# Optimization experiments

Hardware: AMD Instinct MI355X
Metric: run time of the kernel (lower is better)

## Reference

```python
import jax, jax.numpy as jnp
import numpy as np

B, NA, NM, P, IN, H, OUT = 64, 49, 19, 128, 64, 64, 60
H2 = 2 * H  # feature dim after each GCN concat and for the global GAT


def setup_inputs() -> dict:
    key = jax.random.key(0)
    ks = iter(jax.random.split(key, 64))
    def rn(shape, s=0.05):
        return jax.random.normal(next(ks), shape, jnp.float32) * s
    inp = {
        'agent_feature': jax.random.normal(next(ks), (B, NA, IN), jnp.float32),
        'map_feature': jax.random.normal(next(ks), (P, B, NM, IN), jnp.float32),
        'map_mask': jnp.ones((B, P), jnp.int32),
    }
    for pfx in ('a', 'm'):  # agent / map SubNetwork params, 3 layers each
        dims = [IN, H2, H2]
        for i in range(3):
            inp[f'{pfx}w{i}'] = rn((dims[i], H))
            inp[f'{pfx}b{i}'] = jnp.zeros((H,), jnp.float32)
            inp[f'{pfx}g{i}'] = jnp.ones((H,), jnp.float32)   # LayerNorm gamma
            inp[f'{pfx}n{i}'] = jnp.zeros((H,), jnp.float32)  # LayerNorm beta
    inp['gat_fc_w'] = rn((H2, H2))
    inp['gat_attn_w'] = rn((2 * H2,))  # attn_fc over concat([z_src, z_dst])
    inp['mlp_w'] = rn((H2, OUT))
    inp['mlp_b'] = jnp.zeros((OUT,), jnp.float32)
    return inp


def _layer_norm(x, g, b):
    mu = jnp.mean(x, axis=-1, keepdims=True)
    var = jnp.mean((x - mu) ** 2, axis=-1, keepdims=True)
    return g * (x - mu) / jnp.sqrt(var + 1e-5) + b


def _neighbor_max(h):
    # max over all OTHER nodes of a complete digraph (no self loop).
    # top-2 trick per channel avoids materializing an [N,N,D] mailbox.
    top2 = jax.lax.top_k(jnp.swapaxes(h, -1, -2), 2)[0]  # [..., D, 2]
    m1 = top2[..., 0][..., None, :]  # [..., 1, D] global max
    m2 = top2[..., 1][..., None, :]  # [..., 1, D] second max
    return jnp.where(h == m1, m2, m1)


def _subnet(x, params):
    for W, b, g, be in params:
        h = jax.nn.relu(_layer_norm(x @ W + b, g, be))
        x = jnp.concatenate([h, _neighbor_max(h)], axis=-1)
    return x


def _forward(agent_feature, map_feature, ap, mp, gat_fc_w, gat_attn_w, mlp_w, mlp_b):
    a = _subnet(agent_feature, ap)        # [B, NA, 2H]
    m = _subnet(map_feature, mp)          # [P, B, NM, 2H]
    agent_poly = jnp.max(a, axis=1)       # [B, 2H]
    map_poly = jnp.max(m, axis=2)         # [P, B, 2H]
    feats = jnp.concatenate([agent_poly[None], map_poly], axis=0)  # [1+P, B, 2H]
    feats = jnp.swapaxes(feats, 0, 1)     # [B, Nn, 2H], node 0 = agent
    z = feats @ gat_fc_w                  # [B, Nn, 2H]
    s = z @ gat_attn_w[:H2]               # [B, Nn] source contribution
    d = z @ gat_attn_w[H2:]               # [B, Nn] destination contribution
    e = jax.nn.leaky_relu(s[:, :, None] + d[:, None, :], 0.01)  # edge i->j: [B, i, j]
    nn_ = feats.shape[1]
    e = jnp.where(jnp.eye(nn_, dtype=bool)[None], -jnp.inf, e)  # no self edges
    alpha = jax.nn.softmax(e, axis=1)     # segment softmax over sources per dst
    hg = jnp.einsum('bij,bid->bjd', alpha, z)  # weighted-sum message passing
    return hg[:, 0] @ mlp_w + mlp_b       # agent node readout: [B, OUT]


def reference(agent_feature, map_feature, map_mask,
              aw0, ab0, ag0, an0, aw1, ab1, ag1, an1, aw2, ab2, ag2, an2,
              mw0, mb0, mg0, mn0, mw1, mb1, mg1, mn1, mw2, mb2, mg2, mn2,
              gat_fc_w, gat_attn_w, mlp_w, mlp_b):
    del map_mask  # all-ones mask => all P map polylines participate (static)
    ap = [(aw0, ab0, ag0, an0), (aw1, ab1, ag1, an1), (aw2, ab2, ag2, an2)]
    mp = [(mw0, mb0, mg0, mn0), (mw1, mb1, mg1, mn1), (mw2, mb2, mg2, mn2)]
    return _forward(agent_feature, map_feature, ap, mp, gat_fc_w, gat_attn_w, mlp_w, mlp_b)
```

## Files before the change

kernel.cpp:

```cpp
#include <hip/hip_runtime.h>
#include <stdint.h>

#define B_    64
#define NA_   49
#define NM_   19
#define P_    128
#define OUT_  60
#define AGRID 64
#define MGRID 2048
#define XR     96
#define XBYTES (XR * 256)
#define PBYTES (9 * 64 * 4)
#define FEATS_BYTES (129 * 64 * 128 * 4)
#define WT_UINTS_PER_SET 10240

typedef __bf16 bf16x8 __attribute__((ext_vector_type(8)));
typedef float  f32x16 __attribute__((ext_vector_type(16)));
typedef unsigned short ushort_t;

__device__ __forceinline__ unsigned int cvt_pk_bf16(float lo, float hi) {
  unsigned int r;
  asm("v_cvt_pk_bf16_f32 %0, %1, %2" : "=v"(r) : "v"(lo), "v"(hi));
  return r;
}

__device__ __forceinline__ f32x16 zero16() {
  f32x16 z;
#pragma unroll
  for (int i = 0; i < 16; ++i) z[i] = 0.f;
  return z;
}

__device__ __forceinline__ int xswz(int row, int byteoff) {
  return row * 256 + (byteoff ^ ((row & 7) << 4));
}

__global__ void prep_wt(
    const float* __restrict__ aw0, const float* __restrict__ aw1,
    const float* __restrict__ aw2, const float* __restrict__ mw0,
    const float* __restrict__ mw1, const float* __restrict__ mw2,
    unsigned int* __restrict__ dst)
{
  const int U = blockIdx.x * 256 + threadIdx.x;
  const int set = U / WT_UINTS_PER_SET;
  const int u = U - set * WT_UINTS_PER_SET;
  int layer, ul;
  if (u < 2048)      { layer = 0; ul = u; }
  else if (u < 6144) { layer = 1; ul = u - 2048; }
  else               { layer = 2; ul = u - 6144; }
  const float* W;
  if (set == 0) W = (layer == 0) ? aw0 : (layer == 1 ? aw1 : aw2);
  else          W = (layer == 0) ? mw0 : (layer == 1 ? mw1 : mw2);
  int j2 = ul & 3, t = ul >> 2;
  int hi = t & 1; t >>= 1;
  int lr = t & 31; t >>= 5;
  int mt = t & 1;
  int ks = t >> 1;
  int k0 = ks * 16 + hi * 8 + j2 * 2;
  int ch = mt * 32 + lr;
  dst[U] = cvt_pk_bf16(W[k0 * 64 + ch], W[(k0 + 1) * 64 + ch]);
}

template<int KS>
__device__ __forceinline__ void tile_layer(
    const uint4* __restrict__ wt,
    char* __restrict__ xs,
    int xrow0, int vr,
    const float* __restrict__ Pb, const float* __restrict__ Pg,
    const float* __restrict__ Pn)
{
  const int lane = threadIdx.x & 63;
  const int lr   = lane & 31;
  const int hi   = lane >> 5;
  const int ch4  = hi * 4;

  bf16x8 afr[2][KS];
#pragma unroll
  for (int mt = 0; mt < 2; ++mt)
#pragma unroll
    for (int ks = 0; ks < KS; ++ks) {
      union { uint4 u; bf16x8 v; } c;
      c.u = wt[(ks * 2 + mt) * 64 + lr * 2 + hi];
      afr[mt][ks] = c.v;
    }

  const int br = xrow0 + lr;
  f32x16 acc0 = zero16(), acc1 = zero16();
#pragma unroll
  for (int ks = 0; ks < KS; ++ks) {
    bf16x8 bfr = *(const bf16x8*)(xs + xswz(br, ks * 32 + hi * 16));
    acc0 = __builtin_amdgcn_mfma_f32_32x32x16_bf16(afr[0][ks], bfr, acc0, 0, 0, 0);
    acc1 = __builtin_amdgcn_mfma_f32_32x32x16_bf16(afr[1][ks], bfr, acc1, 0, 0, 0);
  }

  float v[2][16];
#pragma unroll
  for (int r = 0; r < 16; ++r) { v[0][r] = acc0[r]; v[1][r] = acc1[r]; }
#pragma unroll
  for (int mt = 0; mt < 2; ++mt)
#pragma unroll
    for (int b = 0; b < 4; ++b) {
      float4 tb = *(const float4*)&Pb[mt * 32 + 8 * b + ch4];
      v[mt][4*b+0] += tb.x; v[mt][4*b+1] += tb.y;
      v[mt][4*b+2] += tb.z; v[mt][4*b+3] += tb.w;
    }
  float s = 0.f, q = 0.f;
#pragma unroll
  for (int r = 0; r < 16; ++r) {
    s += v[0][r] + v[1][r];
    q = fmaf(v[0][r], v[0][r], q);
    q = fmaf(v[1][r], v[1][r], q);
  }
  s += __shfl_xor(s, 32);
  q += __shfl_xor(q, 32);
  float mu   = s * 0.015625f;
  float rstd = rsqrtf(fmaf(q, 0.015625f, -mu * mu) + 1e-5f);

#pragma unroll
  for (int mt = 0; mt < 2; ++mt)
#pragma unroll
    for (int b = 0; b < 4; ++b) {
      float4 tg = *(const float4*)&Pg[mt * 32 + 8 * b + ch4];
      float4 tn = *(const float4*)&Pn[mt * 32 + 8 * b + ch4];
      float h0 = fmaxf(0.f, fmaf((v[mt][4*b+0] - mu) * rstd, tg.x, tn.x));
      float h1 = fmaxf(0.f, fmaf((v[mt][4*b+1] - mu) * rstd, tg.y, tn.y));
      float h2 = fmaxf(0.f, fmaf((v[mt][4*b+2] - mu) * rstd, tg.z, tn.z));
      float h3 = fmaxf(0.f, fmaf((v[mt][4*b+3] - mu) * rstd, tg.w, tn.w));
      uint2 u; u.x = cvt_pk_bf16(h0, h1); u.y = cvt_pk_bf16(h2, h3);
      if (lr < vr)
        *(uint2*)(xs + xswz(br, mt * 64 + 16 * b + 8 * hi)) = u;
    }
}

__device__ __forceinline__ void nmax_map(char* xs) {
  const int tid = threadIdx.x;
  const int g = tid >> 6, c = tid & 63;
  const int rb = g * NM_;
  unsigned int m1 = 0, m2 = 0;
  for (int n = 0; n < NM_; ++n) {
    unsigned int x = *(const ushort_t*)(xs + xswz(rb + n, 2 * c));
    if (x > m1) { m2 = m1; m1 = x; } else if (x > m2) m2 = x;
  }
  for (int n = 0; n < NM_; ++n) {
    unsigned int x = *(const ushort_t*)(xs + xswz(rb + n, 2 * c));
    *(ushort_t*)(xs + xswz(rb + n, 128 + 2 * c)) = (ushort_t)((x == m1) ? m2 : m1);
  }
}

__device__ __forceinline__ void nmax_agent(char* xs) {
  const int tid = threadIdx.x;
  const int c = tid & 63, wid = tid >> 6;
  unsigned int m1 = 0, m2 = 0;
  for (int n = 0; n < NA_; ++n) {
    unsigned int x = *(const ushort_t*)(xs + xswz(n, 2 * c));
    if (x > m1) { m2 = m1; m1 = x; } else if (x > m2) m2 = x;
  }
  int n0 = wid * 13, n1 = (n0 + 13 > NA_) ? NA_ : n0 + 13;
  for (int n = n0; n < n1; ++n) {
    unsigned int x = *(const ushort_t*)(xs + xswz(n, 2 * c));
    *(ushort_t*)(xs + xswz(n, 128 + 2 * c)) = (ushort_t)((x == m1) ? m2 : m1);
  }
}

__device__ __forceinline__ void stage_params(
    const float* b0, const float* g0, const float* n0,
    const float* b1, const float* g1, const float* n1,
    const float* b2, const float* g2, const float* n2, float* Pp)
{
  const int tid = threadIdx.x;
  if (tid < 64) {
    Pp[      tid] = b0[tid]; Pp[ 64 + tid] = g0[tid]; Pp[128 + tid] = n0[tid];
    Pp[192 + tid] = b1[tid]; Pp[256 + tid] = g1[tid]; Pp[320 + tid] = n1[tid];
    Pp[384 + tid] = b2[tid]; Pp[448 + tid] = g2[tid]; Pp[512 + tid] = n2[tid];
  }
}

__global__ __launch_bounds__(256, 4) void subnet3(
    const float* __restrict__ agent, const float* __restrict__ mapf,
    const float* __restrict__ ab0, const float* __restrict__ ag0,
    const float* __restrict__ an0, const float* __restrict__ ab1,
    const float* __restrict__ ag1, const float* __restrict__ an1,
    const float* __restrict__ ab2, const float* __restrict__ ag2,
    const float* __restrict__ an2, const float* __restrict__ mb0,
    const float* __restrict__ mg0, const float* __restrict__ mn0,
    const float* __restrict__ mb1, const float* __restrict__ mg1,
    const float* __restrict__ mn1, const float* __restrict__ mb2,
    const float* __restrict__ mg2, const float* __restrict__ mn2,
    const uint4* __restrict__ wt,
    float* __restrict__ feats)
{
  __shared__ __align__(16) char smem[XBYTES + PBYTES];
  char*  xs = smem;
  float* Pp = (float*)(smem + XBYTES);
  const int tid = threadIdx.x;
  const int wid = tid >> 6;

  if (blockIdx.x < AGRID) {
    const int bid = blockIdx.x;
    for (int i = tid; i < NA_ * 16; i += 256) {
      int row = i >> 4, k4 = (i & 15) * 4;
      float4 v = *(const float4*)&agent[((size_t)bid * NA_ + row) * 64 + k4];
      uint2 u; u.x = cvt_pk_bf16(v.x, v.y); u.y = cvt_pk_bf16(v.z, v.w);
      *(uint2*)(xs + xswz(row, 8 * (i & 15))) = u;
    }
    stage_params(ab0, ag0, an0, ab1, ag1, an1, ab2, ag2, an2, Pp);
    __syncthreads();
    if (wid < 2) tile_layer<4>(wt, xs, wid * 32, wid ? 17 : 32,
                               Pp, Pp + 64, Pp + 128);
    __syncthreads();
    nmax_agent(xs);
    __syncthreads();
    if (wid < 2) tile_layer<8>(wt + 512, xs, wid * 32, wid ? 17 : 32,
                               Pp + 192, Pp + 256, Pp + 320);
    __syncthreads();
    nmax_agent(xs);
    __syncthreads();
    if (wid < 2) tile_layer<8>(wt + 1536, xs, wid * 32, wid ? 17 : 32,
                               Pp + 384, Pp + 448, Pp + 512);
    __syncthreads();
    if (tid < 64) {
      unsigned int m1 = 0;
      for (int n = 0; n < NA_; ++n) {
        unsigned int x = *(const ushort_t*)(xs + xswz(n, 2 * tid));
        m1 = x > m1 ? x : m1;
      }
      float f = __uint_as_float(m1 << 16);
      feats[(size_t)bid * 128 + tid] = f;
      feats[(size_t)bid * 128 + 64 + tid] = f;
    }
  } else {
    const uint4* wtm = wt + 2560;
    const int mbid = blockIdx.x - AGRID;
    const int gbase = mbid * 4;
    for (int i = tid; i < 76 * 16; i += 256) {
      int row = i >> 4, k4 = (i & 15) * 4;
      float4 v = *(const float4*)&mapf[((size_t)gbase * NM_ + row) * 64 + k4];
      uint2 u; u.x = cvt_pk_bf16(v.x, v.y); u.y = cvt_pk_bf16(v.z, v.w);
      *(uint2*)(xs + xswz(row, 8 * (i & 15))) = u;
    }
    stage_params(mb0, mg0, mn0, mb1, mg1, mn1, mb2, mg2, mn2, Pp);
    __syncthreads();
    if (wid < 3) tile_layer<4>(wtm, xs, wid * 32, (wid == 2) ? 12 : 32,
                               Pp, Pp + 64, Pp + 128);
    __syncthreads();
    nmax_map(xs);
    __syncthreads();
    if (wid < 3) tile_layer<8>(wtm + 512, xs, wid * 32, (wid == 2) ? 12 : 32,
                               Pp + 192, Pp + 256, Pp + 320);
    __syncthreads();
    nmax_map(xs);
    __syncthreads();
    if (wid < 3) tile_layer<8>(wtm + 1536, xs, wid * 32, (wid == 2) ? 12 : 32,
                               Pp + 384, Pp + 448, Pp + 512);
    __syncthreads();
    {
      const int g = tid >> 6, c = tid & 63;
      const int rb = g * NM_;
      unsigned int m1 = 0;
      for (int n = 0; n < NM_; ++n) {
        unsigned int x = *(const ushort_t*)(xs + xswz(rb + n, 2 * c));
        m1 = x > m1 ? x : m1;
      }
      float f = __uint_as_float(m1 << 16);
      size_t slot = (size_t)(B_ + gbase + g);
      feats[slot * 128 + c] = f;
      feats[slot * 128 + 64 + c] = f;
    }
  }
}

__global__ __launch_bounds__(256) void gat_kernel(
    const float* __restrict__ feats,
    const float* __restrict__ fcw,
    const float* __restrict__ attnw,
    const float* __restrict__ mlpw,
    const float* __restrict__ mlpb,
    float* __restrict__ out)
{
  const int b = blockIdx.x, tid = threadIdx.x;
  __shared__ float asrc[128], adst[128], was[128], wad[128];
  __shared__ float si[130];
  __shared__ float alpha[128], red[8], ubuf[128], hg[128];

  if (tid < 128) { asrc[tid] = attnw[tid]; adst[tid] = attnw[128 + tid]; }
  __syncthreads();

  if (tid < 128) {
    float s1 = 0.f, s2 = 0.f;
    for (int c = 0; c < 128; ++c) {
      float w = fcw[tid * 128 + c];
      s1 += w * asrc[c];
      s2 += w * adst[c];
    }
    was[tid] = s1; wad[tid] = s2;
  }
  __syncthreads();

  if (tid < 130) {
    const float* wa = (tid == 129) ? wad : was;
    int node = (tid == 129) ? 0 : tid;
    const float* fr = feats + ((size_t)node * B_ + b) * 128;
    float s = 0.f;
    for (int k = 0; k < 128; k += 4) {
      float4 f = *(const float4*)&fr[k];
      s += f.x * wa[k] + f.y * wa[k + 1] + f.z * wa[k + 2] + f.w * wa[k + 3];
    }
    si[tid] = s;
  }
  __syncthreads();

  float d0 = si[129];
  float e = -3.4e38f;
  if (tid < 128) {
    float x = si[tid + 1] + d0;
    e = (x > 0.f) ? x : 0.01f * x;
  }
  float m = e;
#pragma unroll
  for (int off = 32; off; off >>= 1) m = fmaxf(m, __shfl_xor(m, off));
  if ((tid & 63) == 0) red[tid >> 6] = m;
  __syncthreads();
  float mx = fmaxf(red[0], red[1]);
  float p = (tid < 128) ? expf(e - mx) : 0.f;
  float s = p;
#pragma unroll
  for (int off = 32; off; off >>= 1) s += __shfl_xor(s, off);
  if ((tid & 63) == 0) red[4 + (tid >> 6)] = s;
  __syncthreads();
  float denom = red[4] + red[5];
  if (tid < 128) alpha[tid] = p / denom;
  __syncthreads();

  if (tid < 128) {
    float u = 0.f;
    for (int t = 0; t < 128; ++t)
      u += alpha[t] * feats[((size_t)(t + 1) * B_ + b) * 128 + tid];
    ubuf[tid] = u;
  }
  __syncthreads();

  if (tid < 128) {
    float hh = 0.f;
    for (int k = 0; k < 128; ++k) hh += ubuf[k] * fcw[k * 128 + tid];
    hg[tid] = hh;
  }
  __syncthreads();

  if (tid < OUT_) {
    float o = mlpb[tid];
    for (int c = 0; c < 128; ++c) o += hg[c] * mlpw[c * OUT_ + tid];
    out[b * OUT_ + tid] = o;
  }
}

extern "C" void kernel_launch(void* const* d_in, const int* in_sizes, int n_in,
                              void* d_out, int out_size, void* d_ws, size_t ws_size,
                              hipStream_t stream) {
  (void)in_sizes; (void)n_in; (void)out_size; (void)ws_size;

  const float* agent = (const float*)d_in[0];
  const float* mapf  = (const float*)d_in[1];

  const float* aw0 = (const float*)d_in[3];
  const float* ab0 = (const float*)d_in[4];
  const float* ag0 = (const float*)d_in[5];
  const float* an0 = (const float*)d_in[6];
  const float* aw1 = (const float*)d_in[7];
  const float* ab1 = (const float*)d_in[8];
  const float* ag1 = (const float*)d_in[9];
  const float* an1 = (const float*)d_in[10];
  const float* aw2 = (const float*)d_in[11];
  const float* ab2 = (const float*)d_in[12];
  const float* ag2 = (const float*)d_in[13];
  const float* an2 = (const float*)d_in[14];

  const float* mw0 = (const float*)d_in[15];
  const float* mb0 = (const float*)d_in[16];
  const float* mg0 = (const float*)d_in[17];
  const float* mn0 = (const float*)d_in[18];
  const float* mw1 = (const float*)d_in[19];
  const float* mb1 = (const float*)d_in[20];
  const float* mg1 = (const float*)d_in[21];
  const float* mn1 = (const float*)d_in[22];
  const float* mw2 = (const float*)d_in[23];
  const float* mb2 = (const float*)d_in[24];
  const float* mg2 = (const float*)d_in[25];
  const float* mn2 = (const float*)d_in[26];

  const float* fcw   = (const float*)d_in[27];
  const float* attnw = (const float*)d_in[28];
  const float* mlpw  = (const float*)d_in[29];
  const float* mlpb  = (const float*)d_in[30];

  float* feats = (float*)d_ws;
  unsigned int* wt = (unsigned int*)((char*)d_ws + FEATS_BYTES);
  float* out = (float*)d_out;

  prep_wt<<<80, 256, 0, stream>>>(aw0, aw1, aw2, mw0, mw1, mw2, wt);

  subnet3<<<AGRID + MGRID, 256, 0, stream>>>(
      agent, mapf,
      ab0, ag0, an0, ab1, ag1, an1, ab2, ag2, an2,
      mb0, mg0, mn0, mb1, mg1, mn1, mb2, mg2, mn2,
      (const uint4*)wt, feats);

  gat_kernel<<<B_, 256, 0, stream>>>(feats, fcw, attnw, mlpw, mlpb, out);
}
```

Baseline: 59.83 us.

## Give each map polyline its own wave to drop block barriers, hoist GAT weight fold

Map blocks now place each of the 4 polylines in its own 20-row tile handled by one wave (19 valid rows). The layer GEMM, neighbor-max and pooling therefore run wave-locally with no __syncthreads between layers, and all four waves do work instead of three. Launch bounds rise from 4 to 6 blocks per SM. The fcw·attn weight fold moves out of every GAT block into one extra block of the prep kernel, using wave shuffles. The risks are register pressure under the higher occupancy target, and a wasted row in each MFMA tile.

Measured after the change: 98.79 us. +65.1%, slower.

```diff
diff --git a/kernel.cpp b/kernel.cpp
--- a/kernel.cpp
+++ b/kernel.cpp
@@ -11,8 +11,10 @@
 #define XR     96
 #define XBYTES (XR * 256)
 #define PBYTES (9 * 64 * 4)
+#define SMEMB  (XBYTES + PBYTES)
 #define FEATS_BYTES (129 * 64 * 128 * 4)
 #define WT_UINTS_PER_SET 10240
+#define WT_BYTES (2 * WT_UINTS_PER_SET * 4)
 
 typedef __bf16 bf16x8 __attribute__((ext_vector_type(8)));
 typedef float  f32x16 __attribute__((ext_vector_type(16)));
@@ -35,12 +37,30 @@
   return row * 256 + (byteoff ^ ((row & 7) << 4));
 }
 
-__global__ void prep_wt(
+__global__ void prep_kernel(
     const float* __restrict__ aw0, const float* __restrict__ aw1,
     const float* __restrict__ aw2, const float* __restrict__ mw0,
     const float* __restrict__ mw1, const float* __restrict__ mw2,
-    unsigned int* __restrict__ dst)
+    const float* __restrict__ fcw, const float* __restrict__ attnw,
+    unsigned int* __restrict__ dst, float* __restrict__ waswad)
 {
+  if (blockIdx.x == 80) {
+    const int lane = threadIdx.x & 63, wid = threadIdx.x >> 6;
+    float a0 = attnw[lane],       a1 = attnw[64 + lane];
+    float d0 = attnw[128 + lane], d1 = attnw[192 + lane];
+    for (int r = wid; r < 128; r += 4) {
+      float w0 = fcw[r * 128 + lane], w1 = fcw[r * 128 + 64 + lane];
+      float s1 = w0 * a0 + w1 * a1;
+      float s2 = w0 * d0 + w1 * d1;
+#pragma unroll
+      for (int off = 32; off; off >>= 1) {
+        s1 += __shfl_xor(s1, off);
+        s2 += __shfl_xor(s2, off);
+      }
+      if (lane == 0) { waswad[r] = s1; waswad[128 + r] = s2; }
+    }
+    return;
+  }
   const int U = blockIdx.x * 256 + threadIdx.x;
   const int set = U / WT_UINTS_PER_SET;
   const int u = U - set * WT_UINTS_PER_SET;
@@ -63,8 +83,7 @@
 
 template<int KS>
 __device__ __forceinline__ void tile_layer(
-    const uint4* __restrict__ wt,
-    char* __restrict__ xs,
+    const uint4* __restrict__ wt, char* __restrict__ xs,
     int xrow0, int vr,
     const float* __restrict__ Pb, const float* __restrict__ Pg,
     const float* __restrict__ Pn)
@@ -132,19 +151,31 @@
     }
 }
 
-__device__ __forceinline__ void nmax_map(char* xs) {
-  const int tid = threadIdx.x;
-  const int g = tid >> 6, c = tid & 63;
-  const int rb = g * NM_;
+__device__ __forceinline__ void nmax_wave(char* xs, int rb, int nn) {
+  const int lane = threadIdx.x & 63;
   unsigned int m1 = 0, m2 = 0;
-  for (int n = 0; n < NM_; ++n) {
-    unsigned int x = *(const ushort_t*)(xs + xswz(rb + n, 2 * c));
+  for (int n = 0; n < nn; ++n) {
+    unsigned int x = *(const ushort_t*)(xs + xswz(rb + n, 2 * lane));
     if (x > m1) { m2 = m1; m1 = x; } else if (x > m2) m2 = x;
   }
-  for (int n = 0; n < NM_; ++n) {
-    unsigned int x = *(const ushort_t*)(xs + xswz(rb + n, 2 * c));
-    *(ushort_t*)(xs + xswz(rb + n, 128 + 2 * c)) = (ushort_t)((x == m1) ? m2 : m1);
-  }
+  for (int n = 0; n < nn; ++n) {
+    unsigned int x = *(const ushort_t*)(xs + xswz(rb + n, 2 * lane));
+    *(ushort_t*)(xs + xswz(rb + n, 128 + 2 * lane)) =
+        (ushort_t)((x == m1) ? m2 : m1);
+  }
+}
+
+__device__ __forceinline__ void poly_wave(char* xs, int rb, int nn,
+                                          float* __restrict__ dst) {
+  const int lane = threadIdx.x & 63;
+  unsigned int m1 = 0;
+  for (int n = 0; n < nn; ++n) {
+    unsigned int x = *(const ushort_t*)(xs + xswz(rb + n, 2 * lane));
+    m1 = x > m1 ? x : m1;
+  }
+  float f = __uint_as_float(m1 << 16);
+  dst[lane] = f;
+  dst[64 + lane] = f;
 }
 
 __device__ __forceinline__ void nmax_agent(char* xs) {
@@ -175,7 +206,7 @@
   }
 }
 
-__global__ __launch_bounds__(256, 4) void subnet3(
+__global__ __launch_bounds__(256, 6) void subnet4(
     const float* __restrict__ agent, const float* __restrict__ mapf,
     const float* __restrict__ ab0, const float* __restrict__ ag0,
     const float* __restrict__ an0, const float* __restrict__ ab1,
@@ -186,10 +217,9 @@
     const float* __restrict__ mb1, const float* __restrict__ mg1,
     const float* __restrict__ mn1, const float* __restrict__ mb2,
     const float* __restrict__ mg2, const float* __restrict__ mn2,
-    const uint4* __restrict__ wt,
-    float* __restrict__ feats)
+    const uint4* __restrict__ wt, float* __restrict__ feats)
 {
-  __shared__ __align__(16) char smem[XBYTES + PBYTES];
+  __shared__ __align__(16) char smem[SMEMB];
   char*  xs = smem;
   float* Pp = (float*)(smem + XBYTES);
   const int tid = threadIdx.x;
@@ -232,68 +262,41 @@
     const uint4* wtm = wt + 2560;
     const int mbid = blockIdx.x - AGRID;
     const int gbase = mbid * 4;
-    for (int i = tid; i < 76 * 16; i += 256) {
-      int row = i >> 4, k4 = (i & 15) * 4;
-      float4 v = *(const float4*)&mapf[((size_t)gbase * NM_ + row) * 64 + k4];
+    for (int i = tid; i < 4 * NM_ * 16; i += 256) {
+      int g = i / (NM_ * 16);
+      int rem = i - g * (NM_ * 16);
+      int row = rem >> 4, k4 = (rem & 15) * 4;
+      float4 v = *(const float4*)&mapf[((size_t)(gbase + g) * NM_ + row) * 64 + k4];
       uint2 u; u.x = cvt_pk_bf16(v.x, v.y); u.y = cvt_pk_bf16(v.z, v.w);
-      *(uint2*)(xs + xswz(row, 8 * (i & 15))) = u;
+      *(uint2*)(xs + xswz(g * 20 + row, 8 * (rem & 15))) = u;
     }
     stage_params(mb0, mg0, mn0, mb1, mg1, mn1, mb2, mg2, mn2, Pp);
     __syncthreads();
-    if (wid < 3) tile_layer<4>(wtm, xs, wid * 32, (wid == 2) ? 12 : 32,
-                               Pp, Pp + 64, Pp + 128);
-    __syncthreads();
-    nmax_map(xs);
-    __syncthreads();
-    if (wid < 3) tile_layer<8>(wtm + 512, xs, wid * 32, (wid == 2) ? 12 : 32,
-                               Pp + 192, Pp + 256, Pp + 320);
-    __syncthreads();
-    nmax_map(xs);
-    __syncthreads();
-    if (wid < 3) tile_layer<8>(wtm + 1536, xs, wid * 32, (wid == 2) ? 12 : 32,
-                               Pp + 384, Pp + 448, Pp + 512);
-    __syncthreads();
-    {
-      const int g = tid >> 6, c = tid & 63;
-      const int rb = g * NM_;
-      unsigned int m1 = 0;
-      for (int n = 0; n < NM_; ++n) {
-        unsigned int x = *(const ushort_t*)(xs + xswz(rb + n, 2 * c));
-        m1 = x > m1 ? x : m1;
-      }
-      float f = __uint_as_float(m1 << 16);
-      size_t slot = (size_t)(B_ + gbase + g);
-      feats[slot * 128 + c] = f;
-      feats[slot * 128 + 64 + c] = f;
-    }
+
+    const int wb = wid * 20;
+    tile_layer<4>(wtm, xs, wb, NM_, Pp, Pp + 64, Pp + 128);
+    nmax_wave(xs, wb, NM_);
+    tile_layer<8>(wtm + 512, xs, wb, NM_, Pp + 192, Pp + 256, Pp + 320);
+    nmax_wave(xs, wb, NM_);
+    tile_layer<8>(wtm + 1536, xs, wb, NM_, Pp + 384, Pp + 448, Pp + 512);
+    poly_wave(xs, wb, NM_, feats + (size_t)(B_ + gbase + wid) * 128);
   }
 }
 
 __global__ __launch_bounds__(256) void gat_kernel(
     const float* __restrict__ feats,
     const float* __restrict__ fcw,
-    const float* __restrict__ attnw,
+    const float* __restrict__ waswad,
     const float* __restrict__ mlpw,
     const float* __restrict__ mlpb,
     float* __restrict__ out)
 {
   const int b = blockIdx.x, tid = threadIdx.x;
-  __shared__ float asrc[128], adst[128], was[128], wad[128];
+  __shared__ float was[128], wad[128];
   __shared__ float si[130];
   __shared__ float alpha[128], red[8], ubuf[128], hg[128];
 
-  if (tid < 128) { asrc[tid] = attnw[tid]; adst[tid] = attnw[128 + tid]; }
-  __syncthreads();
-
-  if (tid < 128) {
-    float s1 = 0.f, s2 = 0.f;
-    for (int c = 0; c < 128; ++c) {
-      float w = fcw[tid * 128 + c];
-      s1 += w * asrc[c];
-      s2 += w * adst[c];
-    }
-    was[tid] = s1; wad[tid] = s2;
-  }
+  if (tid < 128) { was[tid] = waswad[tid]; wad[tid] = waswad[128 + tid]; }
   __syncthreads();
 
   if (tid < 130) {
@@ -394,15 +397,17 @@
 
   float* feats = (float*)d_ws;
   unsigned int* wt = (unsigned int*)((char*)d_ws + FEATS_BYTES);
+  float* waswad = (float*)((char*)d_ws + FEATS_BYTES + WT_BYTES);
   float* out = (float*)d_out;
 
-  prep_wt<<<80, 256, 0, stream>>>(aw0, aw1, aw2, mw0, mw1, mw2, wt);
-
-  subnet3<<<AGRID + MGRID, 256, 0, stream>>>(
+  prep_kernel<<<81, 256, 0, stream>>>(aw0, aw1, aw2, mw0, mw1, mw2,
+                                      fcw, attnw, wt, waswad);
+
+  subnet4<<<AGRID + MGRID, 256, 0, stream>>>(
       agent, mapf,
       ab0, ag0, an0, ab1, ag1, an1, ab2, ag2, an2,
       mb0, mg0, mn0, mb1, mg1, mn1, mb2, mg2, mn2,
       (const uint4*)wt, feats);
 
-  gat_kernel<<<B_, 256, 0, stream>>>(feats, fcw, attnw, mlpw, mlpb, out);
-}
+  gat_kernel<<<B_, 256, 0, stream>>>(feats, fcw, waswad, mlpw, mlpb, out);
+}
```
